# Optimization experiments

Measured on AMD Instinct MI355X. Metric: run time of the kernel, lower is better.

## Reference

```python
import jax, jax.numpy as jnp
import numpy as np
import math

LN_EPS = 1e-5

def layer_norm(x, g, b):
    mu = jnp.mean(x, axis=-1, keepdims=True)
    var = jnp.mean(jnp.square(x - mu), axis=-1, keepdims=True)
    return (x - mu) * jax.lax.rsqrt(var + LN_EPS) * g + b

def positional_encoding(seq_len, d_model):
    pos = jnp.arange(seq_len, dtype=jnp.float32)[:, None]
    div = jnp.exp(jnp.arange(0, d_model, 2, dtype=jnp.float32) * (-math.log(10000.0) / d_model))
    ang = pos * div  # [S, D/2]
    # interleave: even indices sin, odd indices cos
    return jnp.stack([jnp.sin(ang), jnp.cos(ang)], axis=-1).reshape(seq_len, d_model)

def setup_inputs() -> dict:
    key = jax.random.key(0)
    V, D, H, L, F, B, S = 32000, 768, 12, 6, 3072, 4, 1024
    ks = jax.random.split(key, 12)
    s = 0.02
    inp = {
        'tokens': jax.random.randint(ks[0], (B, S), 0, V),
        'emb': jax.random.normal(ks[1], (V, D), jnp.float32) * s,
        'Wq': jax.random.normal(ks[2], (L, D, D), jnp.float32) * s,
        'bq': jnp.zeros((L, D), jnp.float32),
        'Wk': jax.random.normal(ks[3], (L, D, D), jnp.float32) * s,
        'bk': jnp.zeros((L, D), jnp.float32),
        'Wv': jax.random.normal(ks[4], (L, D, D), jnp.float32) * s,
        'bv': jnp.zeros((L, D), jnp.float32),
        'Wo': jax.random.normal(ks[5], (L, D, D), jnp.float32) * s,
        'bo': jnp.zeros((L, D), jnp.float32),
        'W1': jax.random.normal(ks[6], (L, D, F), jnp.float32) * s,
        'b1': jnp.zeros((L, F), jnp.float32),
        'W2': jax.random.normal(ks[7], (L, F, D), jnp.float32) * s,
        'b2': jnp.zeros((L, D), jnp.float32),
        'ln1_g': jnp.ones((L, D), jnp.float32), 'ln1_b': jnp.zeros((L, D), jnp.float32),
        'ln2_g': jnp.ones((L, D), jnp.float32), 'ln2_b': jnp.zeros((L, D), jnp.float32),
        'lnf_g': jnp.ones((D,), jnp.float32), 'lnf_b': jnp.zeros((D,), jnp.float32),
        'head_W': jax.random.normal(ks[8], (V, D), jnp.float32) * s,
    }
    return inp

def gpt_forward(tokens, emb, Wq, bq, Wk, bk, Wv, bv, Wo, bo, W1, b1, W2, b2,
                ln1_g, ln1_b, ln2_g, ln2_b, lnf_g, lnf_b, head_W):
    B, S = tokens.shape
    D = emb.shape[1]
    H = 12
    dk = D // H
    scale = 1.0 / math.sqrt(dk)
    causal = jnp.tril(jnp.ones((S, S), dtype=bool))  # [S,S]

    x = emb[tokens] + positional_encoding(S, D)  # [B,S,D]

    def block(x, p):
        wq, bq_, wk, bk_, wv, bv_, wo, bo_, w1, b1_, w2, b2_, g1, be1, g2, be2 = p
        h = layer_norm(x, g1, be1)
        q = (h @ wq + bq_).reshape(B, S, H, dk)
        k = (h @ wk + bk_).reshape(B, S, H, dk)
        v = (h @ wv + bv_).reshape(B, S, H, dk)
        scores = jnp.einsum('bqhd,bkhd->bhqk', q, k) * scale
        scores = jnp.where(causal, scores, -jnp.inf)
        attn = jax.nn.softmax(scores, axis=-1)
        o = jnp.einsum('bhqk,bkhd->bqhd', attn, v).reshape(B, S, D)
        x = x + o @ wo + bo_
        h2 = layer_norm(x, g2, be2)
        ff = jax.nn.gelu(h2 @ w1 + b1_, approximate=False) @ w2 + b2_
        x = x + ff
        return x, None

    layer_params = (Wq, bq, Wk, bk, Wv, bv, Wo, bo, W1, b1, W2, b2,
                    ln1_g, ln1_b, ln2_g, ln2_b)
    x, _ = jax.lax.scan(block, x, layer_params)
    x = layer_norm(x, lnf_g, lnf_b)
    logits = jnp.einsum('bsd,vd->bsv', x, head_W)  # head bias=False
    return logits

def reference(tokens, emb, Wq, bq, Wk, bk, Wv, bv, Wo, bo, W1, b1, W2, b2,
              ln1_g, ln1_b, ln2_g, ln2_b, lnf_g, lnf_b, head_W):
    return gpt_forward(tokens, emb, Wq, bq, Wk, bk, Wv, bv, Wo, bo, W1, b1, W2, b2,
                       ln1_g, ln1_b, ln2_g, ln2_b, lnf_g, lnf_b, head_W)
```

## Files before the change

kernel.cpp:

```cpp
#include <hip/hip_runtime.h>
#include <hip/hip_bf16.h>
#include <math.h>

#define BB 4
#define SS 1024
#define DD 768
#define HH 12
#define LL 6
#define FF 3072
#define VV 32000
#define DK 64
#define MM (BB * SS)

typedef __attribute__((ext_vector_type(8))) short s8v;
typedef __attribute__((ext_vector_type(4))) float f4v;

__device__ inline unsigned short f2bf_bits(float f) {
    unsigned u = __builtin_bit_cast(unsigned, f);
    unsigned r = (u + 0x7fffu + ((u >> 16) & 1u)) >> 16;
    return (unsigned short)r;
}

__device__ inline void gl_lds16(const void* g, void* l) {
    __builtin_amdgcn_global_load_lds((const __attribute__((address_space(1))) void*)g,
                                     (__attribute__((address_space(3))) void*)l, 16, 0, 0);
}

__global__ void embed_kernel(const int* __restrict__ tokens,
                             const float* __restrict__ emb,
                             float* __restrict__ x) {
    const int row = blockIdx.x;
    const int s = row % SS;
    const int tok = tokens[row];
    const float* er = emb + (size_t)tok * DD;
    float* xr = x + (size_t)row * DD;
    const float neg_ln_base = -logf(10000.0f) / (float)DD;
    for (int d = threadIdx.x; d < DD; d += blockDim.x) {
        int i2 = d & ~1;
        float div = expf((float)i2 * neg_ln_base);
        float ang = (float)s * div;
        float pe = (d & 1) ? cosf(ang) : sinf(ang);
        xr[d] = er[d] + pe;
    }
}

template <int OUTBF>
__global__ __launch_bounds__(256) void ln_kernel(const float* __restrict__ x,
                                                 const float* __restrict__ g,
                                                 const float* __restrict__ b,
                                                 void* __restrict__ outp) {
    const int row = blockIdx.x;
    const float* xr = x + (size_t)row * DD;
    float s = 0.f, s2 = 0.f;
    for (int d = threadIdx.x; d < DD; d += blockDim.x) {
        float v = xr[d];
        s += v; s2 += v * v;
    }
    __shared__ float rs[4], rs2[4];
    for (int off = 32; off; off >>= 1) {
        s  += __shfl_down(s, off);
        s2 += __shfl_down(s2, off);
    }
    const int wid = threadIdx.x >> 6;
    if ((threadIdx.x & 63) == 0) { rs[wid] = s; rs2[wid] = s2; }
    __syncthreads();
    s  = rs[0] + rs[1] + rs[2] + rs[3];
    s2 = rs2[0] + rs2[1] + rs2[2] + rs2[3];
    const float mu = s / (float)DD;
    const float var = s2 / (float)DD - mu * mu;
    const float r = rsqrtf(var + 1e-5f);
    for (int d = threadIdx.x; d < DD; d += blockDim.x) {
        float v = (xr[d] - mu) * r * g[d] + b[d];
        if (OUTBF) ((unsigned short*)outp)[(size_t)row * DD + d] = f2bf_bits(v);
        else       ((float*)outp)[(size_t)row * DD + d] = v;
    }
}

__global__ __launch_bounds__(256) void prep_kernel(const float* __restrict__ Wq,
                                                   const float* __restrict__ Wk,
                                                   const float* __restrict__ Wv,
                                                   const float* __restrict__ Wo,
                                                   const float* __restrict__ W1,
                                                   const float* __restrict__ W2,
                                                   unsigned short* __restrict__ wqkvT,
                                                   unsigned short* __restrict__ woT,
                                                   unsigned short* __restrict__ w1T,
                                                   unsigned short* __restrict__ w2T) {
    const int id = blockIdx.x;
    const float* src; unsigned short* dst; int R, C, t;
    if (id < 432)       { int seg = id / 144; t = id % 144;
                          src = (seg == 0 ? Wq : seg == 1 ? Wk : Wv);
                          dst = wqkvT + (size_t)seg * DD * DD; R = DD; C = DD; }
    else if (id < 576)  { t = id - 576 + 144; src = Wo; dst = woT; R = DD; C = DD; }
    else if (id < 1152) { t = id - 576;  src = W1; dst = w1T; R = DD; C = FF; }
    else                { t = id - 1152; src = W2; dst = w2T; R = FF; C = DD; }
    const int tilesC = C / 64;
    const int r0 = (t / tilesC) * 64, c0 = (t % tilesC) * 64;
    __shared__ float tb[64][65];
    const int lr = threadIdx.x >> 6, lc = threadIdx.x & 63;
    #pragma unroll
    for (int it = 0; it < 16; ++it) {
        int r = it * 4 + lr;
        tb[r][lc] = src[(size_t)(r0 + r) * C + c0 + lc];
    }
    __syncthreads();
    #pragma unroll
    for (int it = 0; it < 16; ++it) {
        int c = it * 4 + lr;
        dst[(size_t)(c0 + c) * R + r0 + lc] = f2bf_bits(tb[lc][c]);
    }
}

__global__ __launch_bounds__(256) void conv_kernel(const float* __restrict__ in,
                                                   unsigned short* __restrict__ out,
                                                   long n4) {
    long i = (long)blockIdx.x * 256 + threadIdx.x;
    if (i < n4) {
        float4 v = ((const float4*)in)[i];
        ushort4 o;
        o.x = f2bf_bits(v.x); o.y = f2bf_bits(v.y);
        o.z = f2bf_bits(v.z); o.w = f2bf_bits(v.w);
        ((ushort4*)out)[i] = o;
    }
}

template <int ACT, int RES, int OUTMODE>
__global__ __launch_bounds__(256) void gemm_mfma(const unsigned short* __restrict__ A,
                                                 const unsigned short* __restrict__ Bt,
                                                 const float* __restrict__ bias,
                                                 const float* res,
                                                 void* Cout, int M, int N, int K,
                                                 const float* biasK, const float* biasV,
                                                 unsigned short* kout, unsigned short* vtout) {
    __shared__ unsigned short As[128 * 32];
    __shared__ unsigned short Bs[128 * 32];
    const int tid = threadIdx.x;
    const int bm = blockIdx.y * 128, bn = blockIdx.x * 128;
    const int lane = tid & 63;
    const int wave = tid >> 6;
    const int wm = (wave >> 1) * 64, wn = (wave & 1) * 64;

    f4v acc[4][4];
    #pragma unroll
    for (int i = 0; i < 4; i++)
        #pragma unroll
        for (int j = 0; j < 4; j++)
            acc[i][j] = (f4v){0.f, 0.f, 0.f, 0.f};

    const int arow = tid >> 2;
    const int acol = (tid & 3) * 8;
    const unsigned short* gA0 = A  + (size_t)(bm + arow) * K + acol;
    const unsigned short* gA1 = gA0 + (size_t)64 * K;
    const unsigned short* gB0 = Bt + (size_t)(bn + arow) * K + acol;
    const unsigned short* gB1 = gB0 + (size_t)64 * K;
    char* lA0 = (char*)As + tid * 16;
    char* lA1 = lA0 + 4096;
    char* lB0 = (char*)Bs + tid * 16;
    char* lB1 = lB0 + 4096;

    const int fr = lane & 15;
    const int fk = (lane >> 4) * 8;

    for (int k0 = 0; k0 < K; k0 += 32) {
        gl_lds16(gA0 + k0, lA0);
        gl_lds16(gA1 + k0, lA1);
        gl_lds16(gB0 + k0, lB0);
        gl_lds16(gB1 + k0, lB1);
        __syncthreads();
        s8v af[4], bf[4];
        #pragma unroll
        for (int i = 0; i < 4; i++)
            af[i] = *(const s8v*)(As + (wm + i * 16 + fr) * 32 + fk);
        #pragma unroll
        for (int j = 0; j < 4; j++)
            bf[j] = *(const s8v*)(Bs + (wn + j * 16 + fr) * 32 + fk);
        #pragma unroll
        for (int i = 0; i < 4; i++)
            #pragma unroll
            for (int j = 0; j < 4; j++)
                acc[i][j] = __builtin_amdgcn_mfma_f32_16x16x32_bf16(af[i], bf[j], acc[i][j], 0, 0, 0);
        __syncthreads();
    }

    const int r0 = bm + wm + (lane >> 4) * 4;
    const int c0 = bn + wn + fr;
    #pragma unroll
    for (int i = 0; i < 4; i++) {
        const int rb = r0 + i * 16;
        #pragma unroll
        for (int j = 0; j < 4; j++) {
            const int c = c0 + j * 16;
            if (OUTMODE == 3) {
                const int seg = (c >= 1536) ? 2 : (c >= 768 ? 1 : 0);
                const int cc = c - seg * 768;
                const float bb = (seg == 0 ? bias[cc] : seg == 1 ? biasK[cc] : biasV[cc]);
                if (seg < 2) {
                    unsigned short* dst = (seg == 0 ? (unsigned short*)Cout : kout);
                    #pragma unroll
                    for (int q = 0; q < 4; q++)
                        dst[(size_t)(rb + q) * DD + cc] = f2bf_bits(acc[i][j][q] + bb);
                } else {
                    const int b_ = rb / SS, s_ = rb % SS;
                    const int h_ = cc >> 6, dd = cc & 63;
                    ushort4 pk;
                    pk.x = f2bf_bits(acc[i][j][0] + bb);
                    pk.y = f2bf_bits(acc[i][j][1] + bb);
                    pk.z = f2bf_bits(acc[i][j][2] + bb);
                    pk.w = f2bf_bits(acc[i][j][3] + bb);
                    *(ushort4*)(vtout + ((size_t)(b_ * HH + h_) * DK + dd) * SS + s_) = pk;
                }
            } else {
                const float bv = bias ? bias[c] : 0.f;
                #pragma unroll
                for (int q = 0; q < 4; q++) {
                    const int r = rb + q;
                    float v = acc[i][j][q] + bv;
                    if (ACT) v = 0.5f * v * (1.0f + erff(v * 0.70710678118654752f));
                    if (RES) v += res[(size_t)r * N + c];
                    if (OUTMODE == 1) ((unsigned short*)Cout)[(size_t)r * N + c] = f2bf_bits(v);
                    else              ((float*)Cout)[(size_t)r * N + c] = v;
                }
            }
        }
    }
}

__global__ __launch_bounds__(512) void gemm_head(const unsigned short* __restrict__ A,
                                                 const unsigned short* __restrict__ Bt,
                                                 float* __restrict__ C,
                                                 int M, int N, int K) {
    __shared__ unsigned short As[256 * 32];
    __shared__ unsigned short Bs[128 * 32];
    const int tid = threadIdx.x;

    const int nwg = gridDim.x * gridDim.y;
    const int bid = blockIdx.y * gridDim.x + blockIdx.x;
    const int cpx = nwg >> 3;
    const int swz = (bid & 7) * cpx + (bid >> 3);
    const int bx = swz % gridDim.x;
    const int by = swz / gridDim.x;
    const int bm = by * 256, bn = bx * 128;

    const int lane = tid & 63;
    const int wave = tid >> 6;
    const int wm = (wave >> 1) * 64;
    const int wn = (wave & 1) * 64;

    f4v acc[4][4];
    #pragma unroll
    for (int i = 0; i < 4; i++)
        #pragma unroll
        for (int j = 0; j < 4; j++)
            acc[i][j] = (f4v){0.f, 0.f, 0.f, 0.f};

    const int arow = tid >> 2;
    const int acol = (tid & 3) * 8;
    const unsigned short* gA0 = A  + (size_t)(bm + arow) * K + acol;
    const unsigned short* gA1 = gA0 + (size_t)128 * K;
    const unsigned short* gB  = Bt + (size_t)(bn + arow) * K + acol;
    char* lA0 = (char*)As + tid * 16;
    char* lA1 = lA0 + 8192;
    char* lB  = (char*)Bs + tid * 16;

    const int fr = lane & 15;
    const int fk = (lane >> 4) * 8;

    for (int k0 = 0; k0 < K; k0 += 32) {
        gl_lds16(gA0 + k0, lA0);
        gl_lds16(gA1 + k0, lA1);
        gl_lds16(gB + k0, lB);
        __syncthreads();
        s8v af[4], bf[4];
        #pragma unroll
        for (int i = 0; i < 4; i++)
            af[i] = *(const s8v*)(As + (wm + i * 16 + fr) * 32 + fk);
        #pragma unroll
        for (int j = 0; j < 4; j++)
            bf[j] = *(const s8v*)(Bs + (wn + j * 16 + fr) * 32 + fk);
        #pragma unroll
        for (int i = 0; i < 4; i++)
            #pragma unroll
            for (int j = 0; j < 4; j++)
                acc[i][j] = __builtin_amdgcn_mfma_f32_16x16x32_bf16(af[i], bf[j], acc[i][j], 0, 0, 0);
        __syncthreads();
    }

    const int r0 = bm + wm + (lane >> 4) * 4;
    const int c0 = bn + wn + fr;
    #pragma unroll
    for (int i = 0; i < 4; i++) {
        #pragma unroll
        for (int j = 0; j < 4; j++) {
            const int c = c0 + j * 16;
            #pragma unroll
            for (int q = 0; q < 4; q++) {
                const int r = r0 + i * 16 + q;
                __builtin_nontemporal_store(acc[i][j][q], &C[(size_t)r * N + c]);
            }
        }
    }
}

__global__ __launch_bounds__(256) void fattn_kernel(const unsigned short* __restrict__ qb,
                                                    const unsigned short* __restrict__ kb,
                                                    const unsigned short* __restrict__ vt,
                                                    unsigned short* __restrict__ o) {
    __shared__ unsigned short Ks[128 * 64];
    __shared__ unsigned short Vs[64 * 128];
    __shared__ unsigned short Ps[4][16 * 128];

    const int qt = (int)gridDim.x - 1 - (int)blockIdx.x;
    const int bh = blockIdx.y;
    const int b = bh / HH, h = bh % HH;
    const int tid = threadIdx.x;
    const int lane = tid & 63;
    const int w = tid >> 6;
    const int fr = lane & 15;
    const int g  = lane >> 4;

    const int krow_ = tid >> 3;
    const int kcol = (((tid & 7) ^ (krow_ & 7)) * 8);
    const int vrow_ = tid >> 4;
    const int vcol = (((tid & 15) ^ (vrow_ & 7)) * 8);

    const int q0w = qt * 64 + w * 16;
    s8v qf[2];
    {
        const unsigned short* qrow = qb + (size_t)(b * SS + q0w + fr) * DD + h * DK + g * 8;
        qf[0] = *(const s8v*)(qrow);
        qf[1] = *(const s8v*)(qrow + 32);
    }

    f4v ofr[4];
    #pragma unroll
    for (int dj = 0; dj < 4; dj++) ofr[dj] = (f4v){0.f, 0.f, 0.f, 0.f};
    float mrow[4] = {-1e30f, -1e30f, -1e30f, -1e30f};
    float lrow[4] = {0.f, 0.f, 0.f, 0.f};

    unsigned short* Pw = &Ps[w][0];
    const int ktiles = qt / 2 + 1;

    for (int t = 0; t < ktiles; ++t) {
        const int k0 = t * 128;
        #pragma unroll
        for (int i = 0; i < 4; i++) {
            const int r = i * 32 + krow_;
            gl_lds16(kb + (size_t)(b * SS + k0 + r) * DD + h * DK + kcol,
                     (char*)Ks + i * 4096 + tid * 16);
        }
        #pragma unroll
        for (int i = 0; i < 4; i++) {
            const int d = i * 16 + vrow_;
            gl_lds16(vt + ((size_t)bh * DK + d) * SS + k0 + vcol,
                     (char*)Vs + i * 4096 + tid * 16);
        }
        __syncthreads();

        const bool diag = (t == ktiles - 1);
        float p[8][4];
        #pragma unroll
        for (int j = 0; j < 8; j++) {
            const char* kbase = (const char*)Ks + (j * 16 + fr) * 128;
            s8v b0 = *(const s8v*)(kbase + ((g * 16)      ^ ((fr & 7) << 4)));
            s8v b1 = *(const s8v*)(kbase + ((64 + g * 16) ^ ((fr & 7) << 4)));
            f4v a = (f4v){0.f, 0.f, 0.f, 0.f};
            a = __builtin_amdgcn_mfma_f32_16x16x32_bf16(qf[0], b0, a, 0, 0, 0);
            a = __builtin_amdgcn_mfma_f32_16x16x32_bf16(qf[1], b1, a, 0, 0, 0);
            #pragma unroll
            for (int pq = 0; pq < 4; pq++) {
                float sv = a[pq] * 0.125f;
                if (diag && (k0 + j * 16 + fr > q0w + g * 4 + pq)) sv = -1e30f;
                p[j][pq] = sv;
            }
        }

        float rmx[4];
        #pragma unroll
        for (int pq = 0; pq < 4; pq++) {
            float v0 = fmaxf(fmaxf(p[0][pq], p[1][pq]), fmaxf(p[2][pq], p[3][pq]));
            float v1 = fmaxf(fmaxf(p[4][pq], p[5][pq]), fmaxf(p[6][pq], p[7][pq]));
            rmx[pq] = fmaxf(v0, v1);
        }
        #pragma unroll
        for (int off = 1; off < 16; off <<= 1)
            #pragma unroll
            for (int pq = 0; pq < 4; pq++)
                rmx[pq] = fmaxf(rmx[pq], __shfl_xor(rmx[pq], off));

        float mnew[4], scf[4], rsum[4];
        #pragma unroll
        for (int pq = 0; pq < 4; pq++) {
            mnew[pq] = fmaxf(mrow[pq], rmx[pq]);
            scf[pq]  = __expf(mrow[pq] - mnew[pq]);
            rsum[pq] = 0.f;
        }
        #pragma unroll
        for (int j = 0; j < 8; j++)
            #pragma unroll
            for (int pq = 0; pq < 4; pq++) {
                float e = __expf(p[j][pq] - mnew[pq]);
                p[j][pq] = e;
                rsum[pq] += e;
            }
        #pragma unroll
        for (int off = 1; off < 16; off <<= 1)
            #pragma unroll
            for (int pq = 0; pq < 4; pq++)
                rsum[pq] += __shfl_xor(rsum[pq], off);
        #pragma unroll
        for (int pq = 0; pq < 4; pq++) {
            lrow[pq] = lrow[pq] * scf[pq] + rsum[pq];
            mrow[pq] = mnew[pq];
        }
        #pragma unroll
        for (int dj = 0; dj < 4; dj++)
            #pragma unroll
            for (int pq = 0; pq < 4; pq++)
                ofr[dj][pq] *= scf[pq];

        #pragma unroll
        for (int j = 0; j < 8; j++)
            #pragma unroll
            for (int pq = 0; pq < 4; pq++) {
                const int r = g * 4 + pq;
                *(unsigned short*)((char*)Pw + r * 256 +
                                   (((j * 16 + fr) * 2) ^ ((r & 7) << 4))) = f2bf_bits(p[j][pq]);
            }

        s8v pa[4];
        #pragma unroll
        for (int ks = 0; ks < 4; ks++)
            pa[ks] = *(const s8v*)((const char*)Pw + fr * 256 +
                                   ((ks * 64 + g * 16) ^ ((fr & 7) << 4)));
        #pragma unroll
        for (int dj = 0; dj < 4; dj++) {
            const char* vbase = (const char*)Vs + (dj * 16 + fr) * 256;
            #pragma unroll
            for (int ks = 0; ks < 4; ks++) {
                s8v vv = *(const s8v*)(vbase + ((ks * 64 + g * 16) ^ ((fr & 7) << 4)));
                ofr[dj] = __builtin_amdgcn_mfma_f32_16x16x32_bf16(pa[ks], vv, ofr[dj], 0, 0, 0);
            }
        }
        __syncthreads();
    }

    #pragma unroll
    for (int pq = 0; pq < 4; pq++) {
        const float inv = 1.0f / lrow[pq];
        const int row_abs = q0w + g * 4 + pq;
        #pragma unroll
        for (int dj = 0; dj < 4; dj++)
            o[(size_t)(b * SS + row_abs) * DD + h * DK + dj * 16 + fr] =
                f2bf_bits(ofr[dj][pq] * inv);
    }
}

extern "C" void kernel_launch(void* const* d_in, const int* in_sizes, int n_in,
                              void* d_out, int out_size, void* d_ws, size_t ws_size,
                              hipStream_t stream) {
    const int*   tokens = (const int*)d_in[0];
    const float* emb    = (const float*)d_in[1];
    const float* Wq     = (const float*)d_in[2];
    const float* bq     = (const float*)d_in[3];
    const float* Wk     = (const float*)d_in[4];
    const float* bk     = (const float*)d_in[5];
    const float* Wv     = (const float*)d_in[6];
    const float* bv     = (const float*)d_in[7];
    const float* Wo     = (const float*)d_in[8];
    const float* bo     = (const float*)d_in[9];
    const float* W1     = (const float*)d_in[10];
    const float* b1     = (const float*)d_in[11];
    const float* W2     = (const float*)d_in[12];
    const float* b2     = (const float*)d_in[13];
    const float* ln1_g  = (const float*)d_in[14];
    const float* ln1_b  = (const float*)d_in[15];
    const float* ln2_g  = (const float*)d_in[16];
    const float* ln2_b  = (const float*)d_in[17];
    const float* lnf_g  = (const float*)d_in[18];
    const float* lnf_b  = (const float*)d_in[19];
    const float* headW  = (const float*)d_in[20];
    float* out = (float*)d_out;
    (void)in_sizes; (void)n_in; (void)out_size; (void)ws_size;

    const size_t MD  = (size_t)MM * DD;
    const size_t MF  = (size_t)MM * FF;
    const size_t DxD = (size_t)DD * DD;
    const size_t DxF = (size_t)DD * FF;
    const size_t HWs = (size_t)VV * DD;

    char* p = (char*)d_ws;
    float*          x     = (float*)p;          p += MD * 4;
    unsigned short* qb    = (unsigned short*)p; p += MD * 2;
    unsigned short* kbuf  = (unsigned short*)p; p += MD * 2;
    unsigned short* vtb   = (unsigned short*)p; p += MD * 2;
    unsigned short* ao    = (unsigned short*)p; p += MD * 2;
    unsigned short* h     = (unsigned short*)p; p += MD * 2;
    unsigned short* mid   = (unsigned short*)p; p += MF * 2;
    unsigned short* wqkvT = (unsigned short*)p; p += 3 * DxD * 2;
    unsigned short* woT   = (unsigned short*)p; p += DxD * 2;
    unsigned short* w1T   = (unsigned short*)p; p += DxF * 2;
    unsigned short* w2T   = (unsigned short*)p; p += DxF * 2;
    unsigned short* hw    = (unsigned short*)p; p += HWs * 2;

    embed_kernel<<<MM, 256, 0, stream>>>(tokens, emb, x);
    conv_kernel<<<(int)((HWs / 4 + 255) / 256), 256, 0, stream>>>(headW, hw, (long)(HWs / 4));

    const dim3 gQKV(2304 / 128, MM / 128);
    const dim3 gD(DD / 128, MM / 128);
    const dim3 gF(FF / 128, MM / 128);
    const dim3 gHead(VV / 128, MM / 256);
    const dim3 gA(SS / 64, BB * HH);

    for (int l = 0; l < LL; l++) {
        prep_kernel<<<1728, 256, 0, stream>>>(Wq + l * DxD, Wk + l * DxD, Wv + l * DxD,
                                              Wo + l * DxD, W1 + l * DxF, W2 + l * DxF,
                                              wqkvT, woT, w1T, w2T);
        ln_kernel<1><<<MM, 256, 0, stream>>>(x, ln1_g + l * DD, ln1_b + l * DD, h);
        gemm_mfma<0, 0, 3><<<gQKV, 256, 0, stream>>>(h, wqkvT, bq + l * DD, nullptr, qb,
                                                     MM, 2304, DD,
                                                     bk + l * DD, bv + l * DD, kbuf, vtb);
        fattn_kernel<<<gA, 256, 0, stream>>>(qb, kbuf, vtb, ao);
        gemm_mfma<0, 1, 0><<<gD, 256, 0, stream>>>(ao, woT, bo + l * DD, x, x, MM, DD, DD,
                                                   nullptr, nullptr, nullptr, nullptr);
        ln_kernel<1><<<MM, 256, 0, stream>>>(x, ln2_g + l * DD, ln2_b + l * DD, h);
        gemm_mfma<1, 0, 1><<<gF, 256, 0, stream>>>(h, w1T, b1 + l * FF, nullptr, mid,
                                                   MM, FF, DD, nullptr, nullptr, nullptr, nullptr);
        gemm_mfma<0, 1, 0><<<gD, 256, 0, stream>>>(mid, w2T, b2 + l * DD, x, x, MM, DD, FF,
                                                   nullptr, nullptr, nullptr, nullptr);
    }

    ln_kernel<1><<<MM, 256, 0, stream>>>(x, lnf_g, lnf_b, h);
    gemm_head<<<gHead, 512, 0, stream>>>(h, hw, out, MM, VV, DD);
}
```

Before: 1.870 ms.

## Batch weight prep, retile D-output GEMMs, and widen attention query tiles

```diff
diff --git a/kernel.cpp b/kernel.cpp
--- a/kernel.cpp
+++ b/kernel.cpp
@@ -86,14 +86,16 @@
                                                    unsigned short* __restrict__ woT,
                                                    unsigned short* __restrict__ w1T,
                                                    unsigned short* __restrict__ w2T) {
-    const int id = blockIdx.x;
+    const size_t DxD = (size_t)DD * DD, DxF = (size_t)DD * FF;
+    const int lid = blockIdx.x / 1728;
+    const int id  = blockIdx.x % 1728;
     const float* src; unsigned short* dst; int R, C, t;
     if (id < 432)       { int seg = id / 144; t = id % 144;
-                          src = (seg == 0 ? Wq : seg == 1 ? Wk : Wv);
-                          dst = wqkvT + (size_t)seg * DD * DD; R = DD; C = DD; }
-    else if (id < 576)  { t = id - 576 + 144; src = Wo; dst = woT; R = DD; C = DD; }
-    else if (id < 1152) { t = id - 576;  src = W1; dst = w1T; R = DD; C = FF; }
-    else                { t = id - 1152; src = W2; dst = w2T; R = FF; C = DD; }
+                          src = (seg == 0 ? Wq : seg == 1 ? Wk : Wv) + lid * DxD;
+                          dst = wqkvT + lid * 3 * DxD + (size_t)seg * DxD; R = DD; C = DD; }
+    else if (id < 576)  { t = id - 432; src = Wo + lid * DxD; dst = woT + lid * DxD; R = DD; C = DD; }
+    else if (id < 1152) { t = id - 576;  src = W1 + lid * DxF; dst = w1T + lid * DxF; R = DD; C = FF; }
+    else                { t = id - 1152; src = W2 + lid * DxF; dst = w2T + lid * DxF; R = FF; C = DD; }
     const int tilesC = C / 64;
     const int r0 = (t / tilesC) * 64, c0 = (t % tilesC) * 64;
     __shared__ float tb[64][65];
@@ -124,7 +126,7 @@
     }
 }
 
-template <int ACT, int RES, int OUTMODE>
+template <int BM, int BN, int WGM, int WGN, int ACT, int RES, int OUTMODE>
 __global__ __launch_bounds__(256) void gemm_mfma(const unsigned short* __restrict__ A,
                                                  const unsigned short* __restrict__ Bt,
                                                  const float* __restrict__ bias,
@@ -132,63 +134,61 @@
                                                  void* Cout, int M, int N, int K,
                                                  const float* biasK, const float* biasV,
                                                  unsigned short* kout, unsigned short* vtout) {
-    __shared__ unsigned short As[128 * 32];
-    __shared__ unsigned short Bs[128 * 32];
+    __shared__ unsigned short As[BM * 32];
+    __shared__ unsigned short Bs[BN * 32];
+    constexpr int MF = (BM / WGM) / 16;
+    constexpr int NF = (BN / WGN) / 16;
     const int tid = threadIdx.x;
-    const int bm = blockIdx.y * 128, bn = blockIdx.x * 128;
+    const int bm = blockIdx.y * BM, bn = blockIdx.x * BN;
     const int lane = tid & 63;
     const int wave = tid >> 6;
-    const int wm = (wave >> 1) * 64, wn = (wave & 1) * 64;
-
-    f4v acc[4][4];
-    #pragma unroll
-    for (int i = 0; i < 4; i++)
-        #pragma unroll
-        for (int j = 0; j < 4; j++)
+    const int wr = (wave / WGN) * (BM / WGM);
+    const int wc = (wave % WGN) * (BN / WGN);
+
+    f4v acc[MF][NF];
+    #pragma unroll
+    for (int i = 0; i < MF; i++)
+        #pragma unroll
+        for (int j = 0; j < NF; j++)
             acc[i][j] = (f4v){0.f, 0.f, 0.f, 0.f};
 
     const int arow = tid >> 2;
     const int acol = (tid & 3) * 8;
-    const unsigned short* gA0 = A  + (size_t)(bm + arow) * K + acol;
-    const unsigned short* gA1 = gA0 + (size_t)64 * K;
-    const unsigned short* gB0 = Bt + (size_t)(bn + arow) * K + acol;
-    const unsigned short* gB1 = gB0 + (size_t)64 * K;
-    char* lA0 = (char*)As + tid * 16;
-    char* lA1 = lA0 + 4096;
-    char* lB0 = (char*)Bs + tid * 16;
-    char* lB1 = lB0 + 4096;
-
     const int fr = lane & 15;
     const int fk = (lane >> 4) * 8;
 
     for (int k0 = 0; k0 < K; k0 += 32) {
-        gl_lds16(gA0 + k0, lA0);
-        gl_lds16(gA1 + k0, lA1);
-        gl_lds16(gB0 + k0, lB0);
-        gl_lds16(gB1 + k0, lB1);
+        #pragma unroll
+        for (int i = 0; i < BM / 64; i++)
+            gl_lds16(A + (size_t)(bm + i * 64 + arow) * K + k0 + acol,
+                     (char*)As + i * 4096 + tid * 16);
+        #pragma unroll
+        for (int i = 0; i < BN / 64; i++)
+            gl_lds16(Bt + (size_t)(bn + i * 64 + arow) * K + k0 + acol,
+                     (char*)Bs + i * 4096 + tid * 16);
         __syncthreads();
-        s8v af[4], bf[4];
-        #pragma unroll
-        for (int i = 0; i < 4; i++)
-            af[i] = *(const s8v*)(As + (wm + i * 16 + fr) * 32 + fk);
-        #pragma unroll
-        for (int j = 0; j < 4; j++)
-            bf[j] = *(const s8v*)(Bs + (wn + j * 16 + fr) * 32 + fk);
-        #pragma unroll
-        for (int i = 0; i < 4; i++)
-            #pragma unroll
-            for (int j = 0; j < 4; j++)
+        s8v af[MF], bf[NF];
+        #pragma unroll
+        for (int i = 0; i < MF; i++)
+            af[i] = *(const s8v*)(As + (wr + i * 16 + fr) * 32 + fk);
+        #pragma unroll
+        for (int j = 0; j < NF; j++)
+            bf[j] = *(const s8v*)(Bs + (wc + j * 16 + fr) * 32 + fk);
+        #pragma unroll
+        for (int i = 0; i < MF; i++)
+            #pragma unroll
+            for (int j = 0; j < NF; j++)
                 acc[i][j] = __builtin_amdgcn_mfma_f32_16x16x32_bf16(af[i], bf[j], acc[i][j], 0, 0, 0);
         __syncthreads();
     }
 
-    const int r0 = bm + wm + (lane >> 4) * 4;
-    const int c0 = bn + wn + fr;
-    #pragma unroll
-    for (int i = 0; i < 4; i++) {
+    const int r0 = bm + wr + (lane >> 4) * 4;
+    const int c0 = bn + wc + fr;
+    #pragma unroll
+    for (int i = 0; i < MF; i++) {
         const int rb = r0 + i * 16;
         #pragma unroll
-        for (int j = 0; j < 4; j++) {
+        for (int j = 0; j < NF; j++) {
             const int c = c0 + j * 16;
             if (OUTMODE == 3) {
                 const int seg = (c >= 1536) ? 2 : (c >= 768 ? 1 : 0);
@@ -233,12 +233,11 @@
     __shared__ unsigned short Bs[128 * 32];
     const int tid = threadIdx.x;
 
-    const int nwg = gridDim.x * gridDim.y;
-    const int bid = blockIdx.y * gridDim.x + blockIdx.x;
-    const int cpx = nwg >> 3;
-    const int swz = (bid & 7) * cpx + (bid >> 3);
-    const int bx = swz % gridDim.x;
-    const int by = swz / gridDim.x;
+    const int f = blockIdx.y * gridDim.x + blockIdx.x;
+    const int cpx = (gridDim.x * gridDim.y) >> 3;
+    const int virt = (f & 7) * cpx + (f >> 3);
+    const int bx = virt / gridDim.y;
+    const int by = virt % gridDim.y;
     const int bm = by * 256, bn = bx * 128;
 
     const int lane = tid & 63;
@@ -319,26 +318,33 @@
     const int g  = lane >> 4;
 
     const int krow_ = tid >> 3;
-    const int kcol = (((tid & 7) ^ (krow_ & 7)) * 8);
+    const int kcol = ((tid & 7) ^ (krow_ & 7)) * 8;
     const int vrow_ = tid >> 4;
-    const int vcol = (((tid & 15) ^ (vrow_ & 7)) * 8);
-
-    const int q0w = qt * 64 + w * 16;
-    s8v qf[2];
-    {
-        const unsigned short* qrow = qb + (size_t)(b * SS + q0w + fr) * DD + h * DK + g * 8;
-        qf[0] = *(const s8v*)(qrow);
-        qf[1] = *(const s8v*)(qrow + 32);
-    }
-
-    f4v ofr[4];
-    #pragma unroll
-    for (int dj = 0; dj < 4; dj++) ofr[dj] = (f4v){0.f, 0.f, 0.f, 0.f};
-    float mrow[4] = {-1e30f, -1e30f, -1e30f, -1e30f};
-    float lrow[4] = {0.f, 0.f, 0.f, 0.f};
+    const int vcol = ((tid & 15) ^ (vrow_ & 7)) * 8;
+
+    const int q0w = qt * 128 + w * 32;
+    s8v qf[2][2];
+    #pragma unroll
+    for (int ri = 0; ri < 2; ri++) {
+        const unsigned short* qrow =
+            qb + (size_t)(b * SS + q0w + ri * 16 + fr) * DD + h * DK + g * 8;
+        qf[ri][0] = *(const s8v*)(qrow);
+        qf[ri][1] = *(const s8v*)(qrow + 32);
+    }
+
+    f4v ofr[2][4];
+    float mrow[2][4], lrow[2][4];
+    #pragma unroll
+    for (int ri = 0; ri < 2; ri++)
+        #pragma unroll
+        for (int z = 0; z < 4; z++) {
+            ofr[ri][z] = (f4v){0.f, 0.f, 0.f, 0.f};
+            mrow[ri][z] = -1e30f;
+            lrow[ri][z] = 0.f;
+        }
 
     unsigned short* Pw = &Ps[w][0];
-    const int ktiles = qt / 2 + 1;
+    const int ktiles = qt + 1;
 
     for (int t = 0; t < ktiles; ++t) {
         const int k0 = t * 128;
@@ -356,103 +362,108 @@
         }
         __syncthreads();
 
-        const bool diag = (t == ktiles - 1);
-        float p[8][4];
-        #pragma unroll
-        for (int j = 0; j < 8; j++) {
-            const char* kbase = (const char*)Ks + (j * 16 + fr) * 128;
-            s8v b0 = *(const s8v*)(kbase + ((g * 16)      ^ ((fr & 7) << 4)));
-            s8v b1 = *(const s8v*)(kbase + ((64 + g * 16) ^ ((fr & 7) << 4)));
-            f4v a = (f4v){0.f, 0.f, 0.f, 0.f};
-            a = __builtin_amdgcn_mfma_f32_16x16x32_bf16(qf[0], b0, a, 0, 0, 0);
-            a = __builtin_amdgcn_mfma_f32_16x16x32_bf16(qf[1], b1, a, 0, 0, 0);
+        const bool diag = (t == qt);
+        #pragma unroll
+        for (int ri = 0; ri < 2; ri++) {
+            float p[8][4];
+            #pragma unroll
+            for (int j = 0; j < 8; j++) {
+                const char* kbase = (const char*)Ks + (j * 16 + fr) * 128;
+                s8v b0 = *(const s8v*)(kbase + ((g * 16)      ^ ((fr & 7) << 4)));
+                s8v b1 = *(const s8v*)(kbase + ((64 + g * 16) ^ ((fr & 7) << 4)));
+                f4v a = (f4v){0.f, 0.f, 0.f, 0.f};
+                a = __builtin_amdgcn_mfma_f32_16x16x32_bf16(qf[ri][0], b0, a, 0, 0, 0);
+                a = __builtin_amdgcn_mfma_f32_16x16x32_bf16(qf[ri][1], b1, a, 0, 0, 0);
+                #pragma unroll
+                for (int pq = 0; pq < 4; pq++) {
+                    float sv = a[pq] * 0.125f;
+                    if (diag && (j * 16 + fr > w * 32 + ri * 16 + g * 4 + pq)) sv = -1e30f;
+                    p[j][pq] = sv;
+                }
+            }
+
+            float rmx[4];
             #pragma unroll
             for (int pq = 0; pq < 4; pq++) {
-                float sv = a[pq] * 0.125f;
-                if (diag && (k0 + j * 16 + fr > q0w + g * 4 + pq)) sv = -1e30f;
-                p[j][pq] = sv;
-            }
-        }
-
-        float rmx[4];
+                float v0 = fmaxf(fmaxf(p[0][pq], p[1][pq]), fmaxf(p[2][pq], p[3][pq]));
+                float v1 = fmaxf(fmaxf(p[4][pq], p[5][pq]), fmaxf(p[6][pq], p[7][pq]));
+                rmx[pq] = fmaxf(v0, v1);
+            }
+            #pragma unroll
+            for (int off = 1; off < 16; off <<= 1)
+                #pragma unroll
+                for (int pq = 0; pq < 4; pq++)
+                    rmx[pq] = fmaxf(rmx[pq], __shfl_xor(rmx[pq], off));
+
+            float mnew[4], scf[4], rsum[4];
+            #pragma unroll
+            for (int pq = 0; pq < 4; pq++) {
+                mnew[pq] = fmaxf(mrow[ri][pq], rmx[pq]);
+                scf[pq]  = __expf(mrow[ri][pq] - mnew[pq]);
+                rsum[pq] = 0.f;
+            }
+            #pragma unroll
+            for (int j = 0; j < 8; j++)
+                #pragma unroll
+                for (int pq = 0; pq < 4; pq++) {
+                    float e = __expf(p[j][pq] - mnew[pq]);
+                    p[j][pq] = e;
+                    rsum[pq] += e;
+                }
+            #pragma unroll
+            for (int off = 1; off < 16; off <<= 1)
+                #pragma unroll
+                for (int pq = 0; pq < 4; pq++)
+                    rsum[pq] += __shfl_xor(rsum[pq], off);
+            #pragma unroll
+            for (int pq = 0; pq < 4; pq++) {
+                lrow[ri][pq] = lrow[ri][pq] * scf[pq] + rsum[pq];
+                mrow[ri][pq] = mnew[pq];
+            }
+            #pragma unroll
+            for (int dj = 0; dj < 4; dj++)
+                #pragma unroll
+                for (int pq = 0; pq < 4; pq++)
+                    ofr[ri][dj][pq] *= scf[pq];
+
+            #pragma unroll
+            for (int j = 0; j < 8; j++)
+                #pragma unroll
+                for (int pq = 0; pq < 4; pq++) {
+                    const int r = g * 4 + pq;
+                    *(unsigned short*)((char*)Pw + r * 256 +
+                                       (((j * 16 + fr) * 2) ^ ((r & 7) << 4))) = f2bf_bits(p[j][pq]);
+                }
+
+            s8v pa[4];
+            #pragma unroll
+            for (int ks = 0; ks < 4; ks++)
+                pa[ks] = *(const s8v*)((const char*)Pw + fr * 256 +
+                                       ((ks * 64 + g * 16) ^ ((fr & 7) << 4)));
+            #pragma unroll
+            for (int dj = 0; dj < 4; dj++) {
+                const char* vbase = (const char*)Vs + (dj * 16 + fr) * 256;
+                #pragma unroll
+                for (int ks = 0; ks < 4; ks++) {
+                    s8v vv = *(const s8v*)(vbase + ((ks * 64 + g * 16) ^ ((fr & 7) << 4)));
+                    ofr[ri][dj] = __builtin_amdgcn_mfma_f32_16x16x32_bf16(pa[ks], vv, ofr[ri][dj], 0, 0, 0);
+                }
+            }
+        }
+        __syncthreads();
+    }
+
+    #pragma unroll
+    for (int ri = 0; ri < 2; ri++)
         #pragma unroll
         for (int pq = 0; pq < 4; pq++) {
-            float v0 = fmaxf(fmaxf(p[0][pq], p[1][pq]), fmaxf(p[2][pq], p[3][pq]));
-            float v1 = fmaxf(fmaxf(p[4][pq], p[5][pq]), fmaxf(p[6][pq], p[7][pq]));
-            rmx[pq] = fmaxf(v0, v1);
-        }
-        #pragma unroll
-        for (int off = 1; off < 16; off <<= 1)
-            #pragma unroll
-            for (int pq = 0; pq < 4; pq++)
-                rmx[pq] = fmaxf(rmx[pq], __shfl_xor(rmx[pq], off));
-
-        float mnew[4], scf[4], rsum[4];
-        #pragma unroll
-        for (int pq = 0; pq < 4; pq++) {
-            mnew[pq] = fmaxf(mrow[pq], rmx[pq]);
-            scf[pq]  = __expf(mrow[pq] - mnew[pq]);
-            rsum[pq] = 0.f;
-        }
-        #pragma unroll
-        for (int j = 0; j < 8; j++)
-            #pragma unroll
-            for (int pq = 0; pq < 4; pq++) {
-                float e = __expf(p[j][pq] - mnew[pq]);
-                p[j][pq] = e;
-                rsum[pq] += e;
-            }
-        #pragma unroll
-        for (int off = 1; off < 16; off <<= 1)
-            #pragma unroll
-            for (int pq = 0; pq < 4; pq++)
-                rsum[pq] += __shfl_xor(rsum[pq], off);
-        #pragma unroll
-        for (int pq = 0; pq < 4; pq++) {
-            lrow[pq] = lrow[pq] * scf[pq] + rsum[pq];
-            mrow[pq] = mnew[pq];
-        }
-        #pragma unroll
-        for (int dj = 0; dj < 4; dj++)
-            #pragma unroll
-            for (int pq = 0; pq < 4; pq++)
-                ofr[dj][pq] *= scf[pq];
-
-        #pragma unroll
-        for (int j = 0; j < 8; j++)
-            #pragma unroll
-            for (int pq = 0; pq < 4; pq++) {
-                const int r = g * 4 + pq;
-                *(unsigned short*)((char*)Pw + r * 256 +
-                                   (((j * 16 + fr) * 2) ^ ((r & 7) << 4))) = f2bf_bits(p[j][pq]);
-            }
-
-        s8v pa[4];
-        #pragma unroll
-        for (int ks = 0; ks < 4; ks++)
-            pa[ks] = *(const s8v*)((const char*)Pw + fr * 256 +
-                                   ((ks * 64 + g * 16) ^ ((fr & 7) << 4)));
-        #pragma unroll
-        for (int dj = 0; dj < 4; dj++) {
-            const char* vbase = (const char*)Vs + (dj * 16 + fr) * 256;
-            #pragma unroll
-            for (int ks = 0; ks < 4; ks++) {
-                s8v vv = *(const s8v*)(vbase + ((ks * 64 + g * 16) ^ ((fr & 7) << 4)));
-                ofr[dj] = __builtin_amdgcn_mfma_f32_16x16x32_bf16(pa[ks], vv, ofr[dj], 0, 0, 0);
-            }
-        }
-        __syncthreads();
-    }
-
-    #pragma unroll
-    for (int pq = 0; pq < 4; pq++) {
-        const float inv = 1.0f / lrow[pq];
-        const int row_abs = q0w + g * 4 + pq;
-        #pragma unroll
-        for (int dj = 0; dj < 4; dj++)
-            o[(size_t)(b * SS + row_abs) * DD + h * DK + dj * 16 + fr] =
-                f2bf_bits(ofr[dj][pq] * inv);
-    }
+            const float inv = 1.0f / lrow[ri][pq];
+            const int row_abs = q0w + ri * 16 + g * 4 + pq;
+            #pragma unroll
+            for (int dj = 0; dj < 4; dj++)
+                o[(size_t)(b * SS + row_abs) * DD + h * DK + dj * 16 + fr] =
+                    f2bf_bits(ofr[ri][dj][pq] * inv);
+        }
 }
 
 extern "C" void kernel_launch(void* const* d_in, const int* in_sizes, int n_in,
@@ -483,7 +494,7 @@
     (void)in_sizes; (void)n_in; (void)out_size; (void)ws_size;
 
     const size_t MD  = (size_t)MM * DD;
-    const size_t MF  = (size_t)MM * FF;
+    const size_t MF_ = (size_t)MM * FF;
     const size_t DxD = (size_t)DD * DD;
     const size_t DxF = (size_t)DD * FF;
     const size_t HWs = (size_t)VV * DD;
@@ -495,38 +506,39 @@
     unsigned short* vtb   = (unsigned short*)p; p += MD * 2;
     unsigned short* ao    = (unsigned short*)p; p += MD * 2;
     unsigned short* h     = (unsigned short*)p; p += MD * 2;
-    unsigned short* mid   = (unsigned short*)p; p += MF * 2;
-    unsigned short* wqkvT = (unsigned short*)p; p += 3 * DxD * 2;
-    unsigned short* woT   = (unsigned short*)p; p += DxD * 2;
-    unsigned short* w1T   = (unsigned short*)p; p += DxF * 2;
-    unsigned short* w2T   = (unsigned short*)p; p += DxF * 2;
+    unsigned short* mid   = (unsigned short*)p; p += MF_ * 2;
+    unsigned short* wqkvT = (unsigned short*)p; p += 6 * 3 * DxD * 2;
+    unsigned short* woT   = (unsigned short*)p; p += 6 * DxD * 2;
+    unsigned short* w1T   = (unsigned short*)p; p += 6 * DxF * 2;
+    unsigned short* w2T   = (unsigned short*)p; p += 6 * DxF * 2;
     unsigned short* hw    = (unsigned short*)p; p += HWs * 2;
 
     embed_kernel<<<MM, 256, 0, stream>>>(tokens, emb, x);
     conv_kernel<<<(int)((HWs / 4 + 255) / 256), 256, 0, stream>>>(headW, hw, (long)(HWs / 4));
+    prep_kernel<<<6 * 1728, 256, 0, stream>>>(Wq, Wk, Wv, Wo, W1, W2, wqkvT, woT, w1T, w2T);
 
     const dim3 gQKV(2304 / 128, MM / 128);
-    const dim3 gD(DD / 128, MM / 128);
+    const dim3 gDn(DD / 64, MM / 128);
     const dim3 gF(FF / 128, MM / 128);
     const dim3 gHead(VV / 128, MM / 256);
-    const dim3 gA(SS / 64, BB * HH);
+    const dim3 gA(SS / 128, BB * HH);
 
     for (int l = 0; l < LL; l++) {
-        prep_kernel<<<1728, 256, 0, stream>>>(Wq + l * DxD, Wk + l * DxD, Wv + l * DxD,
-                                              Wo + l * DxD, W1 + l * DxF, W2 + l * DxF,
-                                              wqkvT, woT, w1T, w2T);
         ln_kernel<1><<<MM, 256, 0, stream>>>(x, ln1_g + l * DD, ln1_b + l * DD, h);
-        gemm_mfma<0, 0, 3><<<gQKV, 256, 0, stream>>>(h, wqkvT, bq + l * DD, nullptr, qb,
-                                                     MM, 2304, DD,
-                                                     bk + l * DD, bv + l * DD, kbuf, vtb);
+        gemm_mfma<128, 128, 2, 2, 0, 0, 3><<<gQKV, 256, 0, stream>>>(
+            h, wqkvT + (size_t)l * 3 * DxD, bq + l * DD, nullptr, qb, MM, 2304, DD,
+            bk + l * DD, bv + l * DD, kbuf, vtb);
         fattn_kernel<<<gA, 256, 0, stream>>>(qb, kbuf, vtb, ao);
-        gemm_mfma<0, 1, 0><<<gD, 256, 0, stream>>>(ao, woT, bo + l * DD, x, x, MM, DD, DD,
-                                                   nullptr, nullptr, nullptr, nullptr);
+        gemm_mfma<128, 64, 4, 1, 0, 1, 0><<<gDn, 256, 0, stream>>>(
+            ao, woT + (size_t)l * DxD, bo + l * DD, x, x, MM, DD, DD,
+            nullptr, nullptr, nullptr, nullptr);
         ln_kernel<1><<<MM, 256, 0, stream>>>(x, ln2_g + l * DD, ln2_b + l * DD, h);
-        gemm_mfma<1, 0, 1><<<gF, 256, 0, stream>>>(h, w1T, b1 + l * FF, nullptr, mid,
-                                                   MM, FF, DD, nullptr, nullptr, nullptr, nullptr);
-        gemm_mfma<0, 1, 0><<<gD, 256, 0, stream>>>(mid, w2T, b2 + l * DD, x, x, MM, DD, FF,
-                                                   nullptr, nullptr, nullptr, nullptr);
+        gemm_mfma<128, 128, 2, 2, 1, 0, 1><<<gF, 256, 0, stream>>>(
+            h, w1T + (size_t)l * DxF, b1 + l * FF, nullptr, mid, MM, FF, DD,
+            nullptr, nullptr, nullptr, nullptr);
+        gemm_mfma<128, 64, 4, 1, 0, 1, 0><<<gDn, 256, 0, stream>>>(
+            mid, w2T + (size_t)l * DxF, b2 + l * DD, x, x, MM, DD, FF,
+            nullptr, nullptr, nullptr, nullptr);
     }
 
     ln_kernel<1><<<MM, 256, 0, stream>>>(x, lnf_g, lnf_b, h);
```

Measured after the change: 2.068 ms. +10.6%, slower.
